# Performance work log

Measured on AMD Instinct MI355X. Metric: run time of the kernel, lower is better.

Reference implementation:

```python
import jax, jax.numpy as jnp
import numpy as np

BATCH, IN_DIM, OUT_DIM = 512, 1024, 1024

def setup_inputs() -> dict:
    key = jax.random.key(0)
    kx, kw = jax.random.split(key)
    x = jax.random.normal(kx, (BATCH, IN_DIM), dtype=jnp.float32)
    W = jax.random.normal(kw, (OUT_DIM, IN_DIM), dtype=jnp.float32)
    return {"x": x, "W": W}

def reference(x, W):
    # Tropical (max-plus) matmul: y[b,o] = max_i (x[b,i] + W[o,i])
    # x: [B, I], W: [O, I] -> y: [B, O]
    return jnp.max(x[:, None, :] + W[None, :, :], axis=-1)
```

## Files before the change

kernel.cpp:

```cpp
#include <hip/hip_runtime.h>
#include <math.h>


#define MDIM 512
#define NDIM 1024
#define KDIM 1024

#define BM 64
#define BN 64
#define BK 32
#define PAD 4
#define TM 4
#define TN 4
#define NTHREADS 256

__global__ __launch_bounds__(NTHREADS)
void tropical_partial(const float* __restrict__ x, const float* __restrict__ W,
                      float* __restrict__ ws, int KC) {
    __shared__ float As[BK][BM + PAD];
    __shared__ float Bs[BK][BN + PAD];

    const int tiles_n = NDIM / BN;
    const int tile    = blockIdx.x;
    const int tm0     = (tile / tiles_n) * BM;
    const int tn0     = (tile % tiles_n) * BN;
    const int k0      = blockIdx.y * KC;

    const int tid = threadIdx.x;
    const int sm = tid >> 2;
    const int sk = (tid & 3) * 8;
    const int tx = tid & 15;
    const int ty = tid >> 4;

    float acc[TM][TN];
#pragma unroll
    for (int i = 0; i < TM; ++i)
#pragma unroll
        for (int j = 0; j < TN; ++j) acc[i][j] = -INFINITY;

    for (int kt = 0; kt < KC; kt += BK) {
        const int kb = k0 + kt;
        const float4 a0 = *(const float4*)&x[(size_t)(tm0 + sm) * KDIM + kb + sk];
        const float4 a1 = *(const float4*)&x[(size_t)(tm0 + sm) * KDIM + kb + sk + 4];
        const float4 b0 = *(const float4*)&W[(size_t)(tn0 + sm) * KDIM + kb + sk];
        const float4 b1 = *(const float4*)&W[(size_t)(tn0 + sm) * KDIM + kb + sk + 4];

        __syncthreads();
        As[sk + 0][sm] = a0.x; As[sk + 1][sm] = a0.y;
        As[sk + 2][sm] = a0.z; As[sk + 3][sm] = a0.w;
        As[sk + 4][sm] = a1.x; As[sk + 5][sm] = a1.y;
        As[sk + 6][sm] = a1.z; As[sk + 7][sm] = a1.w;
        Bs[sk + 0][sm] = b0.x; Bs[sk + 1][sm] = b0.y;
        Bs[sk + 2][sm] = b0.z; Bs[sk + 3][sm] = b0.w;
        Bs[sk + 4][sm] = b1.x; Bs[sk + 5][sm] = b1.y;
        Bs[sk + 6][sm] = b1.z; Bs[sk + 7][sm] = b1.w;
        __syncthreads();

#pragma unroll 8
        for (int kk = 0; kk < BK; ++kk) {
            const float4 av = *(const float4*)&As[kk][ty * TM];
            const float4 bv = *(const float4*)&Bs[kk][tx * TN];
            const float a[4] = {av.x, av.y, av.z, av.w};
            const float b[4] = {bv.x, bv.y, bv.z, bv.w};
#pragma unroll
            for (int i = 0; i < TM; ++i)
#pragma unroll
                for (int j = 0; j < TN; ++j)
                    acc[i][j] = fmaxf(acc[i][j], a[i] + b[j]);
        }
    }

    float* wsl = ws + (size_t)blockIdx.y * MDIM * NDIM;
#pragma unroll
    for (int i = 0; i < TM; ++i) {
        const float4 v = make_float4(acc[i][0], acc[i][1], acc[i][2], acc[i][3]);
        *(float4*)&wsl[(size_t)(tm0 + ty * TM + i) * NDIM + tn0 + tx * TN] = v;
    }
}

__global__ __launch_bounds__(NTHREADS)
void tropical_reduce(const float* __restrict__ ws, float* __restrict__ out, int KS) {
    const int i = blockIdx.x * NTHREADS + threadIdx.x;
    const int stride = MDIM * NDIM / 4;
    if (i >= stride) return;
    const float4* w4 = (const float4*)ws;
    float4 m = w4[i];
    for (int s = 1; s < KS; ++s) {
        const float4 v = w4[(size_t)s * stride + i];
        m.x = fmaxf(m.x, v.x); m.y = fmaxf(m.y, v.y);
        m.z = fmaxf(m.z, v.z); m.w = fmaxf(m.w, v.w);
    }
    ((float4*)out)[i] = m;
}

extern "C" void kernel_launch(void* const* d_in, const int* in_sizes, int n_in,
                              void* d_out, int out_size, void* d_ws, size_t ws_size,
                              hipStream_t stream) {
    const float* x = (const float*)d_in[0];
    const float* W = (const float*)d_in[1];
    float* out = (float*)d_out;
    float* ws  = (float*)d_ws;

    const size_t slice = (size_t)MDIM * NDIM * sizeof(float);
    int KS = 8;
    while (KS > 1 && (size_t)KS * slice > ws_size) KS >>= 1;

    const int ntiles = (MDIM / BM) * (NDIM / BN);

    if ((size_t)KS * slice > ws_size) {
        tropical_partial<<<dim3(ntiles, 1), NTHREADS, 0, stream>>>(x, W, out, KDIM);
        return;
    }

    const int KC = KDIM / KS;
    tropical_partial<<<dim3(ntiles, KS), NTHREADS, 0, stream>>>(x, W, ws, KC);

    const int nvec4 = MDIM * NDIM / 4;
    tropical_reduce<<<(nvec4 + NTHREADS - 1) / NTHREADS, NTHREADS, 0, stream>>>(ws, out, KS);
}
```

Before: 86.78 us.

## Enlarge M tile to 8x4 per thread, prefetch next K tile, raise split-K

The block tile grows from 64x64 to 128x64, so each thread computes an 8x4 micro-tile, which gives more register reuse per shared-memory load. Global loads for the next K tile are issued before the compute loop so they overlap with the max-plus work. The inner loop is unrolled by two K steps with a fused double fmax, and the split-K factor is doubled to 16 so the grid keeps enough blocks despite the larger tiles. In exchange, register pressure goes up (launch bounds now request 4 blocks) and the reduction kernel has twice as many partial slices to read.

```diff
diff --git a/kernel.cpp b/kernel.cpp
--- a/kernel.cpp
+++ b/kernel.cpp
@@ -6,31 +6,39 @@
 #define NDIM 1024
 #define KDIM 1024
 
-#define BM 64
+#define BM 128
 #define BN 64
 #define BK 32
-#define PAD 4
-#define TM 4
+#define TM 8
 #define TN 4
 #define NTHREADS 256
+#define LDA (BM + 4)
+#define LDB (BN + 4)
 
-__global__ __launch_bounds__(NTHREADS)
+__global__ __launch_bounds__(NTHREADS, 4)
 void tropical_partial(const float* __restrict__ x, const float* __restrict__ W,
                       float* __restrict__ ws, int KC) {
-    __shared__ float As[BK][BM + PAD];
-    __shared__ float Bs[BK][BN + PAD];
+    __shared__ float As[BK][LDA];
+    __shared__ float Bs[BK][LDB];
 
     const int tiles_n = NDIM / BN;
-    const int tile    = blockIdx.x;
-    const int tm0     = (tile / tiles_n) * BM;
-    const int tn0     = (tile % tiles_n) * BN;
-    const int k0      = blockIdx.y * KC;
+    const int tile = blockIdx.x;
+    const int tm0 = (tile / tiles_n) * BM;
+    const int tn0 = (tile % tiles_n) * BN;
+    const int k0  = blockIdx.y * KC;
 
-    const int tid = threadIdx.x;
-    const int sm = tid >> 2;
-    const int sk = (tid & 3) * 8;
-    const int tx = tid & 15;
-    const int ty = tid >> 4;
+    const int t = threadIdx.x;
+
+    const int am = t >> 1;
+    const int ak = (t & 1) * 16;
+    const int bn = t >> 2;
+    const int bk = (t & 3) * 4;
+
+    const float* xp = x + (size_t)(tm0 + am) * KDIM + k0 + ak;
+    const float* wp = W + (size_t)(tn0 + bn) * KDIM + k0 + bk;
+
+    const int ty = t >> 4;
+    const int tx = t & 15;
 
     float acc[TM][TN];
 #pragma unroll
@@ -38,43 +46,65 @@
 #pragma unroll
         for (int j = 0; j < TN; ++j) acc[i][j] = -INFINITY;
 
-    for (int kt = 0; kt < KC; kt += BK) {
-        const int kb = k0 + kt;
-        const float4 a0 = *(const float4*)&x[(size_t)(tm0 + sm) * KDIM + kb + sk];
-        const float4 a1 = *(const float4*)&x[(size_t)(tm0 + sm) * KDIM + kb + sk + 4];
-        const float4 b0 = *(const float4*)&W[(size_t)(tn0 + sm) * KDIM + kb + sk];
-        const float4 b1 = *(const float4*)&W[(size_t)(tn0 + sm) * KDIM + kb + sk + 4];
+    float4 al[4], bl[2];
+    al[0] = *(const float4*)(xp + 0);
+    al[1] = *(const float4*)(xp + 4);
+    al[2] = *(const float4*)(xp + 8);
+    al[3] = *(const float4*)(xp + 12);
+    bl[0] = *(const float4*)(wp + 0);
+    bl[1] = *(const float4*)(wp + 16);
 
+    const int rounds = KC / BK;
+    for (int r = 0; r < rounds; ++r) {
         __syncthreads();
-        As[sk + 0][sm] = a0.x; As[sk + 1][sm] = a0.y;
-        As[sk + 2][sm] = a0.z; As[sk + 3][sm] = a0.w;
-        As[sk + 4][sm] = a1.x; As[sk + 5][sm] = a1.y;
-        As[sk + 6][sm] = a1.z; As[sk + 7][sm] = a1.w;
-        Bs[sk + 0][sm] = b0.x; Bs[sk + 1][sm] = b0.y;
-        Bs[sk + 2][sm] = b0.z; Bs[sk + 3][sm] = b0.w;
-        Bs[sk + 4][sm] = b1.x; Bs[sk + 5][sm] = b1.y;
-        Bs[sk + 6][sm] = b1.z; Bs[sk + 7][sm] = b1.w;
+#pragma unroll
+        for (int q = 0; q < 4; ++q) {
+            As[ak + q * 4 + 0][am] = al[q].x;
+            As[ak + q * 4 + 1][am] = al[q].y;
+            As[ak + q * 4 + 2][am] = al[q].z;
+            As[ak + q * 4 + 3][am] = al[q].w;
+        }
+        Bs[bk + 0][bn] = bl[0].x;  Bs[bk + 1][bn] = bl[0].y;
+        Bs[bk + 2][bn] = bl[0].z;  Bs[bk + 3][bn] = bl[0].w;
+        Bs[bk + 16][bn] = bl[1].x; Bs[bk + 17][bn] = bl[1].y;
+        Bs[bk + 18][bn] = bl[1].z; Bs[bk + 19][bn] = bl[1].w;
         __syncthreads();
 
-#pragma unroll 8
-        for (int kk = 0; kk < BK; ++kk) {
-            const float4 av = *(const float4*)&As[kk][ty * TM];
-            const float4 bv = *(const float4*)&Bs[kk][tx * TN];
-            const float a[4] = {av.x, av.y, av.z, av.w};
-            const float b[4] = {bv.x, bv.y, bv.z, bv.w};
+        if (r + 1 < rounds) {
+            xp += BK; wp += BK;
+            al[0] = *(const float4*)(xp + 0);
+            al[1] = *(const float4*)(xp + 4);
+            al[2] = *(const float4*)(xp + 8);
+            al[3] = *(const float4*)(xp + 12);
+            bl[0] = *(const float4*)(wp + 0);
+            bl[1] = *(const float4*)(wp + 16);
+        }
+
+#pragma unroll
+        for (int kk = 0; kk < BK; kk += 2) {
+            const float4 a00 = *(const float4*)&As[kk][ty * 8];
+            const float4 a01 = *(const float4*)&As[kk][ty * 8 + 4];
+            const float4 a10 = *(const float4*)&As[kk + 1][ty * 8];
+            const float4 a11 = *(const float4*)&As[kk + 1][ty * 8 + 4];
+            const float4 b0v = *(const float4*)&Bs[kk][tx * 4];
+            const float4 b1v = *(const float4*)&Bs[kk + 1][tx * 4];
+            const float a0[8] = {a00.x, a00.y, a00.z, a00.w, a01.x, a01.y, a01.z, a01.w};
+            const float a1[8] = {a10.x, a10.y, a10.z, a10.w, a11.x, a11.y, a11.z, a11.w};
+            const float b0[4] = {b0v.x, b0v.y, b0v.z, b0v.w};
+            const float b1[4] = {b1v.x, b1v.y, b1v.z, b1v.w};
 #pragma unroll
             for (int i = 0; i < TM; ++i)
 #pragma unroll
                 for (int j = 0; j < TN; ++j)
-                    acc[i][j] = fmaxf(acc[i][j], a[i] + b[j]);
+                    acc[i][j] = fmaxf(fmaxf(acc[i][j], a0[i] + b0[j]), a1[i] + b1[j]);
         }
     }
 
-    float* wsl = ws + (size_t)blockIdx.y * MDIM * NDIM;
+    float* o = ws + (size_t)blockIdx.y * MDIM * NDIM;
 #pragma unroll
     for (int i = 0; i < TM; ++i) {
         const float4 v = make_float4(acc[i][0], acc[i][1], acc[i][2], acc[i][3]);
-        *(float4*)&wsl[(size_t)(tm0 + ty * TM + i) * NDIM + tn0 + tx * TN] = v;
+        *(float4*)&o[(size_t)(tm0 + ty * TM + i) * NDIM + tn0 + tx * TN] = v;
     }
 }
 
@@ -102,7 +132,7 @@
     float* ws  = (float*)d_ws;
 
     const size_t slice = (size_t)MDIM * NDIM * sizeof(float);
-    int KS = 8;
+    int KS = 16;
     while (KS > 1 && (size_t)KS * slice > ws_size) KS >>= 1;
 
     const int ntiles = (MDIM / BM) * (NDIM / BN);
```

Result: no change. 87.19 us (+0.5%).

## Replace LDS-tiled max-plus kernel with transposed-x, scalar-broadcast W register kernel

Applied to the files above, without the earlier changes.

Adds a pre-pass that transposes x so each lane reads a coalesced column of x. The partial kernel drops shared-memory tiling; each wave takes 8 W rows, with readfirstlane making the row pointers wave-uniform, and accumulates 8 outputs per lane in registers. Results are staged through LDS so the workspace stores are coalesced. This removes LDS traffic and syncs from the inner loop, but adds a transpose launch, uses more workspace, and gives less reuse per thread (1x8 outputs instead of 4x4), so the kernel leans more on cache bandwidth.

```diff
diff --git a/kernel.cpp b/kernel.cpp
--- a/kernel.cpp
+++ b/kernel.cpp
@@ -5,77 +5,82 @@
 #define MDIM 512
 #define NDIM 1024
 #define KDIM 1024
-
-#define BM 64
-#define BN 64
-#define BK 32
-#define PAD 4
-#define TM 4
-#define TN 4
 #define NTHREADS 256
+#define TN 8
+#define KS_DEF 8
 
 __global__ __launch_bounds__(NTHREADS)
-void tropical_partial(const float* __restrict__ x, const float* __restrict__ W,
+void transpose_x(const float* __restrict__ x, float* __restrict__ xT) {
+    __shared__ float tile[32][33];
+    const int k0 = blockIdx.x * 32;
+    const int m0 = blockIdx.y * 32;
+    const int tx = threadIdx.x & 31;
+    const int ty = threadIdx.x >> 5;
+#pragma unroll
+    for (int i = 0; i < 4; ++i)
+        tile[ty + i * 8][tx] = x[(size_t)(m0 + ty + i * 8) * KDIM + k0 + tx];
+    __syncthreads();
+#pragma unroll
+    for (int i = 0; i < 4; ++i)
+        xT[(size_t)(k0 + ty + i * 8) * MDIM + m0 + tx] = tile[tx][ty + i * 8];
+}
+
+__global__ __launch_bounds__(NTHREADS, 8)
+void tropical_partial(const float* __restrict__ xT, const float* __restrict__ W,
                       float* __restrict__ ws, int KC) {
-    __shared__ float As[BK][BM + PAD];
-    __shared__ float Bs[BK][BN + PAD];
+    const int lane = threadIdx.x & 63;
+    const int wv   = threadIdx.x >> 6;
+    const int mi   = blockIdx.x & 7;
+    const int ni   = blockIdx.x >> 3;
+    const int m0   = mi * 64;
+    const int nc0  = ni * 32;
+    const int nb   = nc0 + wv * TN;
+    const int k0   = blockIdx.y * KC;
 
-    const int tiles_n = NDIM / BN;
-    const int tile    = blockIdx.x;
-    const int tm0     = (tile / tiles_n) * BM;
-    const int tn0     = (tile % tiles_n) * BN;
-    const int k0      = blockIdx.y * KC;
+    const float* wr[TN];
+#pragma unroll
+    for (int j = 0; j < TN; ++j) {
+        const int nu = __builtin_amdgcn_readfirstlane(nb + j);
+        wr[j] = W + (size_t)nu * KDIM + k0;
+    }
+    const float* xp = xT + (size_t)k0 * MDIM + m0 + lane;
 
-    const int tid = threadIdx.x;
-    const int sm = tid >> 2;
-    const int sk = (tid & 3) * 8;
-    const int tx = tid & 15;
-    const int ty = tid >> 4;
+    float acc[TN];
+#pragma unroll
+    for (int j = 0; j < TN; ++j) acc[j] = -INFINITY;
 
-    float acc[TM][TN];
+    for (int kt = 0; kt < KC; kt += 8) {
+        float a[8];
 #pragma unroll
-    for (int i = 0; i < TM; ++i)
+        for (int q = 0; q < 8; ++q)
+            a[q] = xp[(size_t)(kt + q) * MDIM];
+        float4 bv[TN][2];
 #pragma unroll
-        for (int j = 0; j < TN; ++j) acc[i][j] = -INFINITY;
-
-    for (int kt = 0; kt < KC; kt += BK) {
-        const int kb = k0 + kt;
-        const float4 a0 = *(const float4*)&x[(size_t)(tm0 + sm) * KDIM + kb + sk];
-        const float4 a1 = *(const float4*)&x[(size_t)(tm0 + sm) * KDIM + kb + sk + 4];
-        const float4 b0 = *(const float4*)&W[(size_t)(tn0 + sm) * KDIM + kb + sk];
-        const float4 b1 = *(const float4*)&W[(size_t)(tn0 + sm) * KDIM + kb + sk + 4];
-
-        __syncthreads();
-        As[sk + 0][sm] = a0.x; As[sk + 1][sm] = a0.y;
-        As[sk + 2][sm] = a0.z; As[sk + 3][sm] = a0.w;
-        As[sk + 4][sm] = a1.x; As[sk + 5][sm] = a1.y;
-        As[sk + 6][sm] = a1.z; As[sk + 7][sm] = a1.w;
-        Bs[sk + 0][sm] = b0.x; Bs[sk + 1][sm] = b0.y;
-        Bs[sk + 2][sm] = b0.z; Bs[sk + 3][sm] = b0.w;
-        Bs[sk + 4][sm] = b1.x; Bs[sk + 5][sm] = b1.y;
-        Bs[sk + 6][sm] = b1.z; Bs[sk + 7][sm] = b1.w;
-        __syncthreads();
-
-#pragma unroll 8
-        for (int kk = 0; kk < BK; ++kk) {
-            const float4 av = *(const float4*)&As[kk][ty * TM];
-            const float4 bv = *(const float4*)&Bs[kk][tx * TN];
-            const float a[4] = {av.x, av.y, av.z, av.w};
-            const float b[4] = {bv.x, bv.y, bv.z, bv.w};
+        for (int j = 0; j < TN; ++j) {
+            bv[j][0] = *(const float4*)(wr[j] + kt);
+            bv[j][1] = *(const float4*)(wr[j] + kt + 4);
+        }
 #pragma unroll
-            for (int i = 0; i < TM; ++i)
+        for (int j = 0; j < TN; ++j) {
+            const float b[8] = {bv[j][0].x, bv[j][0].y, bv[j][0].z, bv[j][0].w,
+                                bv[j][1].x, bv[j][1].y, bv[j][1].z, bv[j][1].w};
 #pragma unroll
-                for (int j = 0; j < TN; ++j)
-                    acc[i][j] = fmaxf(acc[i][j], a[i] + b[j]);
+            for (int q = 0; q < 8; q += 2)
+                acc[j] = fmaxf(fmaxf(acc[j], a[q] + b[q]), a[q + 1] + b[q + 1]);
         }
     }
 
-    float* wsl = ws + (size_t)blockIdx.y * MDIM * NDIM;
+    __shared__ float st[64][33];
 #pragma unroll
-    for (int i = 0; i < TM; ++i) {
-        const float4 v = make_float4(acc[i][0], acc[i][1], acc[i][2], acc[i][3]);
-        *(float4*)&wsl[(size_t)(tm0 + ty * TM + i) * NDIM + tn0 + tx * TN] = v;
-    }
+    for (int j = 0; j < TN; ++j) st[lane][wv * TN + j] = acc[j];
+    __syncthreads();
+    float* o = ws + (size_t)blockIdx.y * MDIM * NDIM;
+    const int r  = threadIdx.x >> 2;
+    const int c8 = (threadIdx.x & 3) * 8;
+    const float4 v0 = make_float4(st[r][c8 + 0], st[r][c8 + 1], st[r][c8 + 2], st[r][c8 + 3]);
+    const float4 v1 = make_float4(st[r][c8 + 4], st[r][c8 + 5], st[r][c8 + 6], st[r][c8 + 7]);
+    *(float4*)&o[(size_t)(m0 + r) * NDIM + nc0 + c8]     = v0;
+    *(float4*)&o[(size_t)(m0 + r) * NDIM + nc0 + c8 + 4] = v1;
 }
 
 __global__ __launch_bounds__(NTHREADS)
@@ -84,37 +89,51 @@
     const int stride = MDIM * NDIM / 4;
     if (i >= stride) return;
     const float4* w4 = (const float4*)ws;
-    float4 m = w4[i];
+    float4 mv = w4[i];
     for (int s = 1; s < KS; ++s) {
         const float4 v = w4[(size_t)s * stride + i];
-        m.x = fmaxf(m.x, v.x); m.y = fmaxf(m.y, v.y);
-        m.z = fmaxf(m.z, v.z); m.w = fmaxf(m.w, v.w);
+        mv.x = fmaxf(mv.x, v.x); mv.y = fmaxf(mv.y, v.y);
+        mv.z = fmaxf(mv.z, v.z); mv.w = fmaxf(mv.w, v.w);
     }
-    ((float4*)out)[i] = m;
+    ((float4*)out)[i] = mv;
+}
+
+__global__ __launch_bounds__(NTHREADS)
+void tropical_naive(const float* __restrict__ x, const float* __restrict__ W,
+                    float* __restrict__ out) {
+    const int idx = blockIdx.x * NTHREADS + threadIdx.x;
+    const int m = idx >> 10, n = idx & 1023;
+    float acc = -INFINITY;
+    for (int k = 0; k < KDIM; ++k)
+        acc = fmaxf(acc, x[(size_t)m * KDIM + k] + W[(size_t)n * KDIM + k]);
+    out[idx] = acc;
 }
 
 extern "C" void kernel_launch(void* const* d_in, const int* in_sizes, int n_in,
                               void* d_out, int out_size, void* d_ws, size_t ws_size,
                               hipStream_t stream) {
+    (void)in_sizes; (void)n_in; (void)out_size;
     const float* x = (const float*)d_in[0];
     const float* W = (const float*)d_in[1];
     float* out = (float*)d_out;
     float* ws  = (float*)d_ws;
 
-    const size_t slice = (size_t)MDIM * NDIM * sizeof(float);
-    int KS = 8;
-    while (KS > 1 && (size_t)KS * slice > ws_size) KS >>= 1;
+    const size_t elems = (size_t)MDIM * NDIM;
+    int KS = KS_DEF;
+    while (KS > 1 && (1 + (size_t)KS) * elems * 4 > ws_size) KS >>= 1;
 
-    const int ntiles = (MDIM / BM) * (NDIM / BN);
-
-    if ((size_t)KS * slice > ws_size) {
-        tropical_partial<<<dim3(ntiles, 1), NTHREADS, 0, stream>>>(x, W, out, KDIM);
+    if ((1 + (size_t)KS) * elems * 4 > ws_size) {
+        tropical_naive<<<(int)(elems / NTHREADS), NTHREADS, 0, stream>>>(x, W, out);
         return;
     }
 
+    float* xT     = ws;
+    float* slices = ws + elems;
+
+    transpose_x<<<dim3(KDIM / 32, MDIM / 32), NTHREADS, 0, stream>>>(x, xT);
+
     const int KC = KDIM / KS;
-    tropical_partial<<<dim3(ntiles, KS), NTHREADS, 0, stream>>>(x, W, ws, KC);
+    tropical_partial<<<dim3(256, KS), NTHREADS, 0, stream>>>(xT, W, slices, KC);
 
-    const int nvec4 = MDIM * NDIM / 4;
-    tropical_reduce<<<(nvec4 + NTHREADS - 1) / NTHREADS, NTHREADS, 0, stream>>>(ws, out, KS);
+    tropical_reduce<<<(int)(elems / 4 / NTHREADS), NTHREADS, 0, stream>>>(slices, out, KS);
 }
```

Measured after the change: 94.70 us. 1.09x slower.
